# Kernel tuning notes

Measured on AMD Instinct MI355X. Metric: run time of the kernel, lower is better.

## Reference

```python
import jax, jax.numpy as jnp
import numpy as np

V, C, E = 100000, 50000, 1250000
VF, CF, H = 32, 32, 64
ROUNDS = 3


def setup_inputs() -> dict:
    key = jax.random.key(0)
    ks = jax.random.split(key, 16)
    s = lambda d: 1.0 / np.sqrt(d)
    inp = {
        "var_feat": jax.random.normal(ks[0], (V, VF), dtype=jnp.float32),
        "constr_feat": jax.random.normal(ks[1], (C, CF), dtype=jnp.float32),
        "W_var": jax.random.uniform(ks[2], (VF, H), jnp.float32, -s(VF), s(VF)),
        "b_var": jax.random.uniform(ks[3], (H,), jnp.float32, -s(VF), s(VF)),
        "W_con": jax.random.uniform(ks[4], (CF, H), jnp.float32, -s(CF), s(CF)),
        "b_con": jax.random.uniform(ks[5], (H,), jnp.float32, -s(CF), s(CF)),
        "W_v2c": jax.random.uniform(ks[6], (H, H), jnp.float32, -s(H), s(H)),
        "b_v2c": jax.random.uniform(ks[7], (H,), jnp.float32, -s(H), s(H)),
        "W_c2v": jax.random.uniform(ks[8], (H, H), jnp.float32, -s(H), s(H)),
        "b_c2v": jax.random.uniform(ks[9], (H,), jnp.float32, -s(H), s(H)),
        "W_score": jax.random.uniform(ks[10], (H, 1), jnp.float32, -s(H), s(H)),
        "b_score": jax.random.uniform(ks[11], (1,), jnp.float32, -s(H), s(H)),
        "var_idx": jax.random.randint(ks[12], (E,), 0, V, dtype=jnp.int64 if jax.config.jax_enable_x64 else jnp.int32),
        "constr_idx": jax.random.randint(ks[13], (E,), 0, C, dtype=jnp.int64 if jax.config.jax_enable_x64 else jnp.int32),
    }
    return inp


def reference(var_feat, constr_feat, W_var, b_var, W_con, b_con, W_v2c, b_v2c,
              W_c2v, b_c2v, W_score, b_score, var_idx, constr_idx):
    nV = var_feat.shape[0]
    nC = constr_feat.shape[0]
    h_var = jax.nn.relu(var_feat @ W_var + b_var)          # [V, H]
    h_constr = jax.nn.relu(constr_feat @ W_con + b_con)    # [C, H]
    for _ in range(ROUNDS):
        # gather var states along edges, scatter-add into constraint buffer
        msg_c = jax.ops.segment_sum(h_var[var_idx], constr_idx, num_segments=nC)  # [C, H]
        h_constr = jax.nn.relu(h_constr + msg_c @ W_v2c + b_v2c)
        # gather constraint states along edges, scatter-add into variable buffer
        msg_v = jax.ops.segment_sum(h_constr[constr_idx], var_idx, num_segments=nV)  # [V, H]
        h_var = jax.nn.relu(h_var + msg_v @ W_c2v + b_c2v)
    scores = (h_var @ W_score + b_score).reshape(-1)       # [V]
    return scores
```

## Files before the change

### kernel.cpp

```cpp
#include <hip/hip_runtime.h>

typedef unsigned short u16;
typedef unsigned int u32;

#define V_N 100000
#define C_N 50000
#define E_N 1250000
#define VF_N 32
#define H_N 64
#define ROUNDS 3

#define TILE 4096
#define NT ((E_N + TILE - 1) / TILE)
#define NB_C ((C_N + 127) / 128)
#define NB_V ((V_N + 255) / 256)
#define FC_BLOCKS 1280

static __device__ __forceinline__ float bf2f(u16 x) {
  return __uint_as_float(((u32)x) << 16);
}
static __device__ __forceinline__ u16 f2bf(float f) {
  u32 u = __float_as_uint(f);
  u32 r = (u + 0x7fff + ((u >> 16) & 1)) >> 16;
  return (u16)r;
}


__global__ __launch_bounds__(256) void bucket_hist(const int* __restrict__ vi,
                                                   const int* __restrict__ ci,
                                                   int* __restrict__ gh_c,
                                                   int* __restrict__ gh_v) {
  __shared__ int hc[NB_C], hv[NB_V];
  int t = threadIdx.x;
  for (int j = t; j < NB_C; j += 256) hc[j] = 0;
  for (int j = t; j < NB_V; j += 256) hv[j] = 0;
  __syncthreads();
  int base = blockIdx.x * TILE;
#pragma unroll
  for (int i = 0; i < 16; ++i) {
    int idx = base + i * 256 + t;
    if (idx < E_N) {
      atomicAdd(&hc[ci[idx] >> 7], 1);
      atomicAdd(&hv[vi[idx] >> 8], 1);
    }
  }
  __syncthreads();
  for (int j = t; j < NB_C; j += 256) if (hc[j]) atomicAdd(&gh_c[j], hc[j]);
  for (int j = t; j < NB_V; j += 256) if (hv[j]) atomicAdd(&gh_v[j], hv[j]);
}

__global__ __launch_bounds__(512) void bucket_scan(const int* __restrict__ gh_c,
                                                   const int* __restrict__ gh_v,
                                                   int* __restrict__ base_c,
                                                   int* __restrict__ cursor_c,
                                                   int* __restrict__ base_v,
                                                   int* __restrict__ cursor_v,
                                                   int* __restrict__ rs_c,
                                                   int* __restrict__ rs_v) {
  __shared__ int lds[512];
  int t = threadIdx.x;
  int x = (t < NB_C) ? gh_c[t] : 0;
  lds[t] = x;
  __syncthreads();
  for (int off = 1; off < 512; off <<= 1) {
    int v = (t >= off) ? lds[t - off] : 0;
    __syncthreads();
    lds[t] += v;
    __syncthreads();
  }
  int excl = lds[t] - x;
  if (t < NB_C) { base_c[t] = excl; cursor_c[t] = excl; }
  if (t == 511) base_c[NB_C] = lds[511];
  __syncthreads();
  int y = (t < NB_V) ? gh_v[t] : 0;
  lds[t] = y;
  __syncthreads();
  for (int off = 1; off < 512; off <<= 1) {
    int v = (t >= off) ? lds[t - off] : 0;
    __syncthreads();
    lds[t] += v;
    __syncthreads();
  }
  int excl2 = lds[t] - y;
  if (t < NB_V) { base_v[t] = excl2; cursor_v[t] = excl2; }
  if (t == 511) base_v[NB_V] = lds[511];
  if (t == 0) { rs_c[C_N] = E_N; rs_v[V_N] = E_N; }
}

__global__ __launch_bounds__(256) void scatter_pack(const int* __restrict__ vi,
                                                    const int* __restrict__ ci,
                                                    int* __restrict__ cursor_c,
                                                    int* __restrict__ cursor_v,
                                                    int* __restrict__ packed_c,
                                                    int* __restrict__ packed_v) {
  __shared__ int hc[NB_C], hv[NB_V], sc[NB_C], sv[NB_V];
  int t = threadIdx.x;
  for (int j = t; j < NB_C; j += 256) hc[j] = 0;
  for (int j = t; j < NB_V; j += 256) hv[j] = 0;
  __syncthreads();
  int base = blockIdx.x * TILE;
  int cc[16], vv[16];
#pragma unroll
  for (int i = 0; i < 16; ++i) {
    int idx = base + i * 256 + t;
    if (idx < E_N) {
      cc[i] = ci[idx];
      vv[i] = vi[idx];
      atomicAdd(&hc[cc[i] >> 7], 1);
      atomicAdd(&hv[vv[i] >> 8], 1);
    } else {
      cc[i] = -1;
      vv[i] = -1;
    }
  }
  __syncthreads();
  for (int j = t; j < NB_C; j += 256) {
    int n = hc[j];
    if (n > 0) sc[j] = atomicAdd(&cursor_c[j], n);
    hc[j] = 0;
  }
  for (int j = t; j < NB_V; j += 256) {
    int n = hv[j];
    if (n > 0) sv[j] = atomicAdd(&cursor_v[j], n);
    hv[j] = 0;
  }
  __syncthreads();
#pragma unroll
  for (int i = 0; i < 16; ++i) {
    if (cc[i] >= 0) {
      int b = cc[i] >> 7;
      int r = atomicAdd(&hc[b], 1);
      packed_c[sc[b] + r] = ((cc[i] & 127) << 17) | vv[i];
      int b2 = vv[i] >> 8;
      int r2 = atomicAdd(&hv[b2], 1);
      packed_v[sv[b2] + r2] = ((vv[i] & 255) << 17) | cc[i];
    }
  }
}

template <int LOCAL_N, int N_DEST>
__global__ __launch_bounds__(256) void fine_sort(const int* __restrict__ packed,
                                                 const int* __restrict__ base,
                                                 int* __restrict__ rs,
                                                 int* __restrict__ srco) {
  __shared__ int cnt[LOCAL_N];
  __shared__ int excl[LOCAL_N];
  int b = blockIdx.x, t = threadIdx.x;
  int s0 = base[b], s1 = base[b + 1];
  if (t < LOCAL_N) cnt[t] = 0;
  __syncthreads();
  for (int i = s0 + t; i < s1; i += 256) atomicAdd(&cnt[packed[i] >> 17], 1);
  __syncthreads();
  if (t == 0) {
    int run = 0;
    for (int k = 0; k < LOCAL_N; ++k) { excl[k] = run; run += cnt[k]; }
  }
  __syncthreads();
  if (t < LOCAL_N) {
    int d = b * LOCAL_N + t;
    if (d < N_DEST) rs[d] = s0 + excl[t];
    cnt[t] = excl[t];
  }
  __syncthreads();
  for (int i = s0 + t; i < s1; i += 256) {
    int w = packed[i];
    int ld = w >> 17;
    int pos = s0 + atomicAdd(&cnt[ld], 1);
    srco[pos] = w & 0x1FFFF;
  }
}


template <int WRITE_BF>
__global__ __launch_bounds__(256) void init_mlp(const float* __restrict__ feat,
                                                const float* __restrict__ W,
                                                const float* __restrict__ b,
                                                float* __restrict__ h,
                                                u16* __restrict__ hbf, int n) {
  __shared__ float Wl[VF_N * H_N];
  for (int i = threadIdx.x; i < VF_N * H_N; i += 256) Wl[i] = W[i];
  __syncthreads();
  int g = (blockIdx.x * 256 + threadIdx.x) >> 4;
  int lane = threadIdx.x & 15;
  if (g >= n) return;
  float2 rv = *(const float2*)&feat[(size_t)g * VF_N + lane * 2];
  float4 acc = *(const float4*)&b[lane * 4];
#pragma unroll
  for (int k = 0; k < VF_N; ++k) {
    float el = (k & 1) ? rv.y : rv.x;
    float v = __shfl(el, k >> 1, 16);
    float4 w = *(const float4*)&Wl[k * H_N + lane * 4];
    acc.x += v * w.x; acc.y += v * w.y; acc.z += v * w.z; acc.w += v * w.w;
  }
  acc.x = fmaxf(acc.x, 0.f); acc.y = fmaxf(acc.y, 0.f);
  acc.z = fmaxf(acc.z, 0.f); acc.w = fmaxf(acc.w, 0.f);
  *(float4*)&h[(size_t)g * H_N + lane * 4] = acc;
  if (WRITE_BF) {
    ushort4 q;
    q.x = f2bf(acc.x); q.y = f2bf(acc.y); q.z = f2bf(acc.z); q.w = f2bf(acc.w);
    *(ushort4*)&hbf[(size_t)g * H_N + lane * 4] = q;
  }
}


static __device__ __forceinline__ void gather_rows_bf16(const u16* __restrict__ tbl,
                                                        const int* __restrict__ src,
                                                        int s, int e, int lane,
                                                        float4& acc) {
  int p = s;
  for (; p + 16 <= e; p += 16) {
    int myidx = src[p + lane];
    ushort4 vv[16];
#pragma unroll
    for (int j = 0; j < 16; ++j) {
      int sj = __shfl(myidx, j, 16);
      vv[j] = *(const ushort4*)&tbl[(size_t)sj * H_N + lane * 4];
    }
#pragma unroll
    for (int j = 0; j < 16; ++j) {
      acc.x += bf2f(vv[j].x); acc.y += bf2f(vv[j].y);
      acc.z += bf2f(vv[j].z); acc.w += bf2f(vv[j].w);
    }
  }
  if (p < e) {
    int cnt = e - p;
    int myidx = (lane < cnt) ? src[p + lane] : 0;
    ushort4 vv[16];
#pragma unroll
    for (int j = 0; j < 16; ++j) {
      int sj = __shfl(myidx, j, 16);
      vv[j] = *(const ushort4*)&tbl[(size_t)sj * H_N + lane * 4];
    }
#pragma unroll
    for (int j = 0; j < 16; ++j) {
      if (j < cnt) {
        acc.x += bf2f(vv[j].x); acc.y += bf2f(vv[j].y);
        acc.z += bf2f(vv[j].z); acc.w += bf2f(vv[j].w);
      }
    }
  }
}


__global__ __launch_bounds__(256) void fused_c(const u16* __restrict__ h_var_bf,
                                               const int* __restrict__ rs,
                                               const int* __restrict__ src,
                                               const float* __restrict__ W1g,
                                               const float* __restrict__ b1g,
                                               const float* __restrict__ W2g,
                                               float* __restrict__ h_con,
                                               u16* __restrict__ t_out) {
  __shared__ float W1[H_N * H_N];
  __shared__ float W2[H_N * H_N];
  for (int i = threadIdx.x; i < H_N * H_N; i += 256) { W1[i] = W1g[i]; W2[i] = W2g[i]; }
  __syncthreads();
  int lane = threadIdx.x & 15;
  int grp = threadIdx.x >> 4;
  for (int g0 = blockIdx.x * 16; g0 < C_N; g0 += FC_BLOCKS * 16) {
    int g = g0 + grp;
    if (g >= C_N) continue;
    int s = rs[g], e = rs[g + 1];
    float4 acc = {0.f, 0.f, 0.f, 0.f};
    gather_rows_bf16(h_var_bf, src, s, e, lane, acc);
    float4 m = {0.f, 0.f, 0.f, 0.f};
#pragma unroll
    for (int k = 0; k < H_N; ++k) {
      int sel = k & 3;
      float el = (sel == 0) ? acc.x : (sel == 1) ? acc.y : (sel == 2) ? acc.z : acc.w;
      float v = __shfl(el, k >> 2, 16);
      float4 w = *(const float4*)&W1[k * H_N + lane * 4];
      m.x += v * w.x; m.y += v * w.y; m.z += v * w.z; m.w += v * w.w;
    }
    float4 hv = *(const float4*)&h_con[(size_t)g * H_N + lane * 4];
    float4 b4 = *(const float4*)&b1g[lane * 4];
    float4 hn;
    hn.x = fmaxf(hv.x + m.x + b4.x, 0.f);
    hn.y = fmaxf(hv.y + m.y + b4.y, 0.f);
    hn.z = fmaxf(hv.z + m.z + b4.z, 0.f);
    hn.w = fmaxf(hv.w + m.w + b4.w, 0.f);
    *(float4*)&h_con[(size_t)g * H_N + lane * 4] = hn;
    float4 tt = {0.f, 0.f, 0.f, 0.f};
#pragma unroll
    for (int k = 0; k < H_N; ++k) {
      int sel = k & 3;
      float el = (sel == 0) ? hn.x : (sel == 1) ? hn.y : (sel == 2) ? hn.z : hn.w;
      float v = __shfl(el, k >> 2, 16);
      float4 w = *(const float4*)&W2[k * H_N + lane * 4];
      tt.x += v * w.x; tt.y += v * w.y; tt.z += v * w.z; tt.w += v * w.w;
    }
    ushort4 q;
    q.x = f2bf(tt.x); q.y = f2bf(tt.y); q.z = f2bf(tt.z); q.w = f2bf(tt.w);
    *(ushort4*)&t_out[(size_t)g * H_N + lane * 4] = q;
  }
}


template <int DO_SCORE>
__global__ __launch_bounds__(256) void gather_v_k(const u16* __restrict__ t,
                                                  const int* __restrict__ rs,
                                                  const int* __restrict__ src,
                                                  const float* __restrict__ bias,
                                                  float* __restrict__ h,
                                                  u16* __restrict__ hbf,
                                                  const float* __restrict__ Ws,
                                                  const float* __restrict__ bs,
                                                  float* __restrict__ out) {
  int g = (blockIdx.x * 256 + threadIdx.x) >> 4;
  int lane = threadIdx.x & 15;
  if (g >= V_N) return;
  int s = rs[g], e = rs[g + 1];
  float4 acc = {0.f, 0.f, 0.f, 0.f};
  gather_rows_bf16(t, src, s, e, lane, acc);
  float4 hv = *(const float4*)&h[(size_t)g * H_N + lane * 4];
  float4 b4 = *(const float4*)&bias[lane * 4];
  float4 hn;
  hn.x = fmaxf(hv.x + acc.x + b4.x, 0.f);
  hn.y = fmaxf(hv.y + acc.y + b4.y, 0.f);
  hn.z = fmaxf(hv.z + acc.z + b4.z, 0.f);
  hn.w = fmaxf(hv.w + acc.w + b4.w, 0.f);
  if (DO_SCORE) {
    float4 w = *(const float4*)&Ws[lane * 4];
    float d = hn.x * w.x + hn.y * w.y + hn.z * w.z + hn.w * w.w;
    d += __shfl_down(d, 8, 16);
    d += __shfl_down(d, 4, 16);
    d += __shfl_down(d, 2, 16);
    d += __shfl_down(d, 1, 16);
    if (lane == 0) out[g] = d + bs[0];
  } else {
    *(float4*)&h[(size_t)g * H_N + lane * 4] = hn;
    ushort4 q;
    q.x = f2bf(hn.x); q.y = f2bf(hn.y); q.z = f2bf(hn.z); q.w = f2bf(hn.w);
    *(ushort4*)&hbf[(size_t)g * H_N + lane * 4] = q;
  }
}


extern "C" void kernel_launch(void* const* d_in, const int* in_sizes, int n_in,
                              void* d_out, int out_size, void* d_ws, size_t ws_size,
                              hipStream_t stream) {
  const float* var_feat = (const float*)d_in[0];
  const float* con_feat = (const float*)d_in[1];
  const float* W_var = (const float*)d_in[2];
  const float* b_var = (const float*)d_in[3];
  const float* W_con = (const float*)d_in[4];
  const float* b_con = (const float*)d_in[5];
  const float* W_v2c = (const float*)d_in[6];
  const float* b_v2c = (const float*)d_in[7];
  const float* W_c2v = (const float*)d_in[8];
  const float* b_c2v = (const float*)d_in[9];
  const float* W_score = (const float*)d_in[10];
  const float* b_score = (const float*)d_in[11];
  const int* var_idx = (const int*)d_in[12];
  const int* constr_idx = (const int*)d_in[13];
  float* out = (float*)d_out;

  char* p = (char*)d_ws;
  auto alloc = [&](size_t bytes) {
    char* r = p;
    p += (bytes + 255) & ~(size_t)255;
    return r;
  };
  float* h_var = (float*)alloc((size_t)V_N * H_N * 4);
  u16* h_var_bf = (u16*)alloc((size_t)V_N * H_N * 2);
  float* h_con = (float*)alloc((size_t)C_N * H_N * 4);
  u16* t_bf = (u16*)alloc((size_t)C_N * H_N * 2);
  int* rs_c = (int*)alloc((size_t)(C_N + 1) * 4);
  int* rs_v = (int*)alloc((size_t)(V_N + 1) * 4);
  int* src_c = (int*)alloc((size_t)E_N * 4);
  int* src_v = (int*)alloc((size_t)E_N * 4);
  int* packed_c = (int*)alloc((size_t)E_N * 4);
  int* packed_v = (int*)alloc((size_t)E_N * 4);
  int* ghist_c = (int*)alloc((size_t)NB_C * 4);
  int* ghist_v = (int*)alloc((size_t)NB_V * 4);
  int* base_c = (int*)alloc((size_t)(NB_C + 1) * 4);
  int* base_v = (int*)alloc((size_t)(NB_V + 1) * 4);
  int* cursor_c = (int*)alloc((size_t)NB_C * 4);
  int* cursor_v = (int*)alloc((size_t)NB_V * 4);

  hipMemsetAsync(ghist_c, 0, (size_t)NB_C * 4, stream);
  hipMemsetAsync(ghist_v, 0, (size_t)NB_V * 4, stream);

  bucket_hist<<<NT, 256, 0, stream>>>(var_idx, constr_idx, ghist_c, ghist_v);
  bucket_scan<<<1, 512, 0, stream>>>(ghist_c, ghist_v, base_c, cursor_c,
                                     base_v, cursor_v, rs_c, rs_v);
  scatter_pack<<<NT, 256, 0, stream>>>(var_idx, constr_idx, cursor_c, cursor_v,
                                       packed_c, packed_v);
  fine_sort<128, C_N><<<NB_C, 256, 0, stream>>>(packed_c, base_c, rs_c, src_c);
  fine_sort<256, V_N><<<NB_V, 256, 0, stream>>>(packed_v, base_v, rs_v, src_v);

  init_mlp<1><<<(V_N + 15) / 16, 256, 0, stream>>>(var_feat, W_var, b_var, h_var, h_var_bf, V_N);
  init_mlp<0><<<(C_N + 15) / 16, 256, 0, stream>>>(con_feat, W_con, b_con, h_con, nullptr, C_N);

  for (int r = 0; r < ROUNDS; ++r) {
    fused_c<<<FC_BLOCKS, 256, 0, stream>>>(h_var_bf, rs_c, src_c,
                                           W_v2c, b_v2c, W_c2v, h_con, t_bf);
    if (r < ROUNDS - 1) {
      gather_v_k<0><<<(V_N + 15) / 16, 256, 0, stream>>>(t_bf, rs_v, src_v, b_c2v, h_var,
                                                         h_var_bf, nullptr, nullptr, nullptr);
    } else {
      gather_v_k<1><<<(V_N + 15) / 16, 256, 0, stream>>>(t_bf, rs_v, src_v, b_c2v, h_var,
                                                         nullptr, W_score, b_score, out);
    }
  }
}
```

Before: 333.5 us.

## Use bf16 MFMA with hi/lo split for constraint-side dense transforms

Replaces the shuffle-based FP32 64x64 matmuls in the constraint update kernel with MFMA 16x16x32 bf16 instructions. Both activations and weights are split into high and low bf16 parts and combined with three MFMAs to stay close to fp32 accuracy. A new prep kernel transposes and splits the weights once, and each wave stages its 16-row tile through padded LDS planes. The block count is also lowered. This adds LDS traffic and conversion work, while the kernel may still be bound by the gather.

```diff
diff --git a/kernel.cpp b/kernel.cpp
--- a/kernel.cpp
+++ b/kernel.cpp
@@ -2,6 +2,8 @@
 
 typedef unsigned short u16;
 typedef unsigned int u32;
+typedef __attribute__((ext_vector_type(8))) short short8v;
+typedef __attribute__((ext_vector_type(4))) float f32x4;
 
 #define V_N 100000
 #define C_N 50000
@@ -14,7 +16,8 @@
 #define NT ((E_N + TILE - 1) / TILE)
 #define NB_C ((C_N + 127) / 128)
 #define NB_V ((V_N + 255) / 256)
-#define FC_BLOCKS 1280
+#define FC_BLOCKS 768
+#define KPAD 72
 
 static __device__ __forceinline__ float bf2f(u16 x) {
   return __uint_as_float(((u32)x) << 16);
@@ -171,6 +174,25 @@
 }
 
 
+__global__ __launch_bounds__(256) void prep_w(const float* __restrict__ W1,
+                                              const float* __restrict__ W2,
+                                              u16* __restrict__ wp) {
+  int i = blockIdx.x * 256 + threadIdx.x;
+  if (i >= H_N * H_N) return;
+  int k = i >> 6, n = i & 63;
+  float w1 = W1[i];
+  u16 h1 = f2bf(w1);
+  u16 l1 = f2bf(w1 - bf2f(h1));
+  wp[(0 * 64 + n) * 64 + k] = h1;
+  wp[(1 * 64 + n) * 64 + k] = l1;
+  float w2 = W2[i];
+  u16 h2 = f2bf(w2);
+  u16 l2 = f2bf(w2 - bf2f(h2));
+  wp[(2 * 64 + n) * 64 + k] = h2;
+  wp[(3 * 64 + n) * 64 + k] = l2;
+}
+
+
 template <int WRITE_BF>
 __global__ __launch_bounds__(256) void init_mlp(const float* __restrict__ feat,
                                                 const float* __restrict__ W,
@@ -245,52 +267,105 @@
 __global__ __launch_bounds__(256) void fused_c(const u16* __restrict__ h_var_bf,
                                                const int* __restrict__ rs,
                                                const int* __restrict__ src,
-                                               const float* __restrict__ W1g,
+                                               const u16* __restrict__ wp,
                                                const float* __restrict__ b1g,
-                                               const float* __restrict__ W2g,
                                                float* __restrict__ h_con,
                                                u16* __restrict__ t_out) {
-  __shared__ float W1[H_N * H_N];
-  __shared__ float W2[H_N * H_N];
-  for (int i = threadIdx.x; i < H_N * H_N; i += 256) { W1[i] = W1g[i]; W2[i] = W2g[i]; }
-  __syncthreads();
+  __shared__ u16 Wlds[4 * 64 * 64];
+  __shared__ u16 Aplanes[4][2 * 16 * KPAD];
+
+  for (int i = threadIdx.x; i < 4 * 64 * 64 / 2; i += 256)
+    ((u32*)Wlds)[i] = ((const u32*)wp)[i];
+  __syncthreads();
+
+  int lane64 = threadIdx.x & 63;
+  int wave = threadIdx.x >> 6;
   int lane = threadIdx.x & 15;
-  int grp = threadIdx.x >> 4;
-  for (int g0 = blockIdx.x * 16; g0 < C_N; g0 += FC_BLOCKS * 16) {
-    int g = g0 + grp;
-    if (g >= C_N) continue;
-    int s = rs[g], e = rs[g + 1];
-    float4 acc = {0.f, 0.f, 0.f, 0.f};
-    gather_rows_bf16(h_var_bf, src, s, e, lane, acc);
-    float4 m = {0.f, 0.f, 0.f, 0.f};
-#pragma unroll
-    for (int k = 0; k < H_N; ++k) {
-      int sel = k & 3;
-      float el = (sel == 0) ? acc.x : (sel == 1) ? acc.y : (sel == 2) ? acc.z : acc.w;
-      float v = __shfl(el, k >> 2, 16);
-      float4 w = *(const float4*)&W1[k * H_N + lane * 4];
-      m.x += v * w.x; m.y += v * w.y; m.z += v * w.z; m.w += v * w.w;
-    }
-    float4 hv = *(const float4*)&h_con[(size_t)g * H_N + lane * 4];
-    float4 b4 = *(const float4*)&b1g[lane * 4];
-    float4 hn;
-    hn.x = fmaxf(hv.x + m.x + b4.x, 0.f);
-    hn.y = fmaxf(hv.y + m.y + b4.y, 0.f);
-    hn.z = fmaxf(hv.z + m.z + b4.z, 0.f);
-    hn.w = fmaxf(hv.w + m.w + b4.w, 0.f);
-    *(float4*)&h_con[(size_t)g * H_N + lane * 4] = hn;
-    float4 tt = {0.f, 0.f, 0.f, 0.f};
-#pragma unroll
-    for (int k = 0; k < H_N; ++k) {
-      int sel = k & 3;
-      float el = (sel == 0) ? hn.x : (sel == 1) ? hn.y : (sel == 2) ? hn.z : hn.w;
-      float v = __shfl(el, k >> 2, 16);
-      float4 w = *(const float4*)&W2[k * H_N + lane * 4];
-      tt.x += v * w.x; tt.y += v * w.y; tt.z += v * w.z; tt.w += v * w.w;
-    }
-    ushort4 q;
-    q.x = f2bf(tt.x); q.y = f2bf(tt.y); q.z = f2bf(tt.z); q.w = f2bf(tt.w);
-    *(ushort4*)&t_out[(size_t)g * H_N + lane * 4] = q;
+  int grp = (threadIdx.x >> 4) & 3;
+  int arow = lane64 & 15;
+  int kq = lane64 >> 4;
+  u16* P = &Aplanes[wave][0];
+
+  float bias[4];
+#pragma unroll
+  for (int nt = 0; nt < 4; ++nt) bias[nt] = b1g[nt * 16 + arow];
+
+  for (int base = (blockIdx.x * 4 + wave) * 16; base < C_N;
+       base += FC_BLOCKS * 4 * 16) {
+    for (int q = 0; q < 4; ++q) {
+      int row = 4 * q + grp;
+      int g = base + row;
+      float4 acc = {0.f, 0.f, 0.f, 0.f};
+      if (g < C_N) gather_rows_bf16(h_var_bf, src, rs[g], rs[g + 1], lane, acc);
+      ushort4 qh, ql;
+      qh.x = f2bf(acc.x); ql.x = f2bf(acc.x - bf2f(qh.x));
+      qh.y = f2bf(acc.y); ql.y = f2bf(acc.y - bf2f(qh.y));
+      qh.z = f2bf(acc.z); ql.z = f2bf(acc.z - bf2f(qh.z));
+      qh.w = f2bf(acc.w); ql.w = f2bf(acc.w - bf2f(qh.w));
+      *(ushort4*)&P[0 * 16 * KPAD + row * KPAD + lane * 4] = qh;
+      *(ushort4*)&P[1 * 16 * KPAD + row * KPAD + lane * 4] = ql;
+    }
+    asm volatile("" ::: "memory");
+    short8v A1h[2], A1l[2];
+#pragma unroll
+    for (int ks = 0; ks < 2; ++ks) {
+      A1h[ks] = *(const short8v*)&P[0 * 16 * KPAD + arow * KPAD + ks * 32 + kq * 8];
+      A1l[ks] = *(const short8v*)&P[1 * 16 * KPAD + arow * KPAD + ks * 32 + kq * 8];
+    }
+    asm volatile("" ::: "memory");
+#pragma unroll
+    for (int nt = 0; nt < 4; ++nt) {
+      int bcol = nt * 16 + arow;
+      f32x4 c = {0.f, 0.f, 0.f, 0.f};
+#pragma unroll
+      for (int ks = 0; ks < 2; ++ks) {
+        short8v Bh = *(const short8v*)&Wlds[(0 * 64 + bcol) * 64 + ks * 32 + kq * 8];
+        short8v Bl = *(const short8v*)&Wlds[(1 * 64 + bcol) * 64 + ks * 32 + kq * 8];
+        c = __builtin_amdgcn_mfma_f32_16x16x32_bf16(A1h[ks], Bh, c, 0, 0, 0);
+        c = __builtin_amdgcn_mfma_f32_16x16x32_bf16(A1l[ks], Bh, c, 0, 0, 0);
+        c = __builtin_amdgcn_mfma_f32_16x16x32_bf16(A1h[ks], Bl, c, 0, 0, 0);
+      }
+#pragma unroll
+      for (int r = 0; r < 4; ++r) {
+        int row = kq * 4 + r;
+        int g = base + row;
+        float hv = (g < C_N) ? h_con[(size_t)g * H_N + nt * 16 + arow] : 0.f;
+        float hn = fmaxf(hv + c[r] + bias[nt], 0.f);
+        if (g < C_N) h_con[(size_t)g * H_N + nt * 16 + arow] = hn;
+        u16 hi = f2bf(hn);
+        u16 lo = f2bf(hn - bf2f(hi));
+        P[0 * 16 * KPAD + row * KPAD + nt * 16 + arow] = hi;
+        P[1 * 16 * KPAD + row * KPAD + nt * 16 + arow] = lo;
+      }
+    }
+    asm volatile("" ::: "memory");
+    short8v A2h[2], A2l[2];
+#pragma unroll
+    for (int ks = 0; ks < 2; ++ks) {
+      A2h[ks] = *(const short8v*)&P[0 * 16 * KPAD + arow * KPAD + ks * 32 + kq * 8];
+      A2l[ks] = *(const short8v*)&P[1 * 16 * KPAD + arow * KPAD + ks * 32 + kq * 8];
+    }
+    asm volatile("" ::: "memory");
+#pragma unroll
+    for (int nt = 0; nt < 4; ++nt) {
+      int bcol = nt * 16 + arow;
+      f32x4 c = {0.f, 0.f, 0.f, 0.f};
+#pragma unroll
+      for (int ks = 0; ks < 2; ++ks) {
+        short8v Bh = *(const short8v*)&Wlds[(2 * 64 + bcol) * 64 + ks * 32 + kq * 8];
+        short8v Bl = *(const short8v*)&Wlds[(3 * 64 + bcol) * 64 + ks * 32 + kq * 8];
+        c = __builtin_amdgcn_mfma_f32_16x16x32_bf16(A2h[ks], Bh, c, 0, 0, 0);
+        c = __builtin_amdgcn_mfma_f32_16x16x32_bf16(A2l[ks], Bh, c, 0, 0, 0);
+        c = __builtin_amdgcn_mfma_f32_16x16x32_bf16(A2h[ks], Bl, c, 0, 0, 0);
+      }
+#pragma unroll
+      for (int r = 0; r < 4; ++r) {
+        int row = kq * 4 + r;
+        int g = base + row;
+        if (g < C_N) t_out[(size_t)g * H_N + nt * 16 + arow] = f2bf(c[r]);
+      }
+    }
+    asm volatile("" ::: "memory");
   }
 }
 
@@ -364,6 +439,7 @@
   u16* h_var_bf = (u16*)alloc((size_t)V_N * H_N * 2);
   float* h_con = (float*)alloc((size_t)C_N * H_N * 4);
   u16* t_bf = (u16*)alloc((size_t)C_N * H_N * 2);
+  u16* wp = (u16*)alloc((size_t)4 * 64 * 64 * 2);
   int* rs_c = (int*)alloc((size_t)(C_N + 1) * 4);
   int* rs_v = (int*)alloc((size_t)(V_N + 1) * 4);
   int* src_c = (int*)alloc((size_t)E_N * 4);
@@ -388,12 +464,14 @@
   fine_sort<128, C_N><<<NB_C, 256, 0, stream>>>(packed_c, base_c, rs_c, src_c);
   fine_sort<256, V_N><<<NB_V, 256, 0, stream>>>(packed_v, base_v, rs_v, src_v);
 
+  prep_w<<<(H_N * H_N + 255) / 256, 256, 0, stream>>>(W_v2c, W_c2v, wp);
+
   init_mlp<1><<<(V_N + 15) / 16, 256, 0, stream>>>(var_feat, W_var, b_var, h_var, h_var_bf, V_N);
   init_mlp<0><<<(C_N + 15) / 16, 256, 0, stream>>>(con_feat, W_con, b_con, h_con, nullptr, C_N);
 
   for (int r = 0; r < ROUNDS; ++r) {
-    fused_c<<<FC_BLOCKS, 256, 0, stream>>>(h_var_bf, rs_c, src_c,
-                                           W_v2c, b_v2c, W_c2v, h_con, t_bf);
+    fused_c<<<FC_BLOCKS, 256, 0, stream>>>(h_var_bf, rs_c, src_c, wp,
+                                           b_v2c, h_con, t_bf);
     if (r < ROUNDS - 1) {
       gather_v_k<0><<<(V_N + 15) / 16, 256, 0, stream>>>(t_bf, rs_v, src_v, b_c2v, h_var,
                                                          h_var_bf, nullptr, nullptr, nullptr);
```

Measured after the change: 345.2 us. +3.5%, slower.
